# Kernel optimization log

Hardware: AMD Instinct MI355X
Metric: run time of the kernel (lower is better)

Reference implementation:

```python
import jax, jax.numpy as jnp
import numpy as np

CHANNEL = 512
EDGE_F = 30
NB, NA = 16, 128


def setup_inputs() -> dict:
    key = jax.random.key(0)
    ks = jax.random.split(key, 8)
    h = jax.random.normal(ks[0], (NB, NA, CHANNEL), dtype=jnp.float32)
    e = jax.random.normal(ks[1], (NB, NA, NA, EDGE_F), dtype=jnp.float32)
    node_mask = jax.random.randint(ks[2], (NB, NA, 1), 0, 2).astype(jnp.float32)
    edge_mask = jax.random.randint(ks[3], (NB, NA, NA, 1), 0, 2).astype(jnp.float32)
    # Linear params (torch convention: y = x @ W.T + b), kaiming-uniform-ish scale
    lim_f = 1.0 / np.sqrt(EDGE_F)
    filter_W = jax.random.uniform(ks[4], (CHANNEL, EDGE_F), jnp.float32, -lim_f, lim_f)
    filter_b = jax.random.uniform(ks[5], (CHANNEL,), jnp.float32, -lim_f, lim_f)
    lim_w = 1.0 / np.sqrt(2 * CHANNEL)
    w_W = jax.random.uniform(ks[6], (CHANNEL, 2 * CHANNEL), jnp.float32, -lim_w, lim_w)
    w_b = jax.random.uniform(ks[7], (CHANNEL,), jnp.float32, -lim_w, lim_w)
    return {"h": h, "e": e, "node_mask": node_mask, "edge_mask": edge_mask,
            "filter_W": filter_W, "filter_b": filter_b, "w_W": w_W, "w_b": w_b}


def reference(h, e, node_mask, edge_mask, filter_W, filter_b, w_W, w_b):
    # edge filter: Linear(30 -> C) + SELU, masked  -> (n_b, n_a, n_a, C)
    ef = jax.nn.selu(jnp.einsum('bijf,cf->bijc', e, filter_W) + filter_b) * edge_mask
    # h1[b,i,c] = sum_j h[b,j,c] * ef[b,i,j,c]   (masked sum aggregation)
    h1 = jnp.einsum('bjc,bijc->bic', h, ef)
    # node MLP on concat([h, h1]) + SELU, masked, residual
    z = jnp.concatenate([h, h1], axis=-1)  # (n_b, n_a, 2C)
    h1 = jax.nn.selu(jnp.einsum('bid,cd->bic', z, w_W) + w_b) * node_mask
    return h1 + h
```

## Files before the change

### kernel.cpp

```cpp
#include <hip/hip_runtime.h>
#include <hip/hip_bf16.h>
#include <math.h>

#define NBATCH 16
#define NA     128
#define CH     512
#define EFEAT  30

typedef __attribute__((ext_vector_type(8))) short          bf16x8;
typedef __attribute__((ext_vector_type(4))) float          f32x4;
typedef __attribute__((ext_vector_type(8))) unsigned short ushort8;
typedef __attribute__((ext_vector_type(4))) unsigned short ushort4_t;

__device__ __forceinline__ float selu_f(float x) {
    const float SA = 1.7580993408473766f;
    float e = __expf(x);
    return x > 0.0f ? 1.0507009873554805f * x : fmaf(SA, e, -SA);
}

__device__ __forceinline__ unsigned short f2bf(float f) {
    __hip_bfloat16 h = __float2bfloat16(f);
    return *reinterpret_cast<unsigned short*>(&h);
}

__global__ __launch_bounds__(256, 4)
void k_edge_mfma(const float* __restrict__ h, const float* __restrict__ e,
                 const float* __restrict__ node_mask, const float* __restrict__ edge_mask,
                 const float* __restrict__ fW, const float* __restrict__ fb,
                 unsigned short* __restrict__ z)
{
    __shared__ unsigned short e_lds[NA * 40];
    __shared__ int   jlist[NA];
    __shared__ int   wcnt[2];

    const int row = (blockIdx.x & 7) * 256 + (blockIdx.x >> 3);
    if (node_mask[row] == 0.0f) return;
    const int b = row >> 7;

    const int tid  = threadIdx.x;
    const int lane = tid & 63;
    const int wv   = tid >> 6;
    const int s    = lane & 15;
    const int g    = lane >> 4;
    const int cbase = wv * 128;

    float myq = 0.0f; unsigned long long bl = 0;
    if (tid < NA) {
        myq = edge_mask[(size_t)row * NA + tid];
        bl = __ballot(myq != 0.0f);
        if ((tid & 63) == 0) wcnt[tid >> 6] = __popcll(bl);
    }
    __syncthreads();
    const int nlive  = wcnt[0] + wcnt[1];
    const int ntiles = (nlive + 15) >> 4;
    if (tid < NA) {
        if (myq != 0.0f) {
            const int base = (tid >= 64) ? wcnt[0] : 0;
            const int pos  = __popcll(bl & ((1ull << (tid & 63)) - 1));
            jlist[base + pos] = tid;
        }
        if (tid >= nlive) jlist[tid] = 0;
    }
    __syncthreads();

    bf16x8 afrag[8];
    #pragma unroll
    for (int cf = 0; cf < 8; ++cf) {
        const int c = cbase + cf * 16 + s;
        const float* wrow = fW + (size_t)c * EFEAT;
        ushort8 t;
        #pragma unroll
        for (int e8 = 0; e8 < 8; ++e8) {
            const int k = g * 8 + e8;
            const float v = (k < EFEAT) ? wrow[k] : (k == EFEAT ? fb[c] : 0.0f);
            t[e8] = f2bf(v);
        }
        afrag[cf] = *(bf16x8*)&t;
    }

    const float* esrc = e + (size_t)row * (NA * EFEAT);
    const int npad = ntiles * 16;
    for (int idx = tid; idx < npad * 32; idx += 256) {
        const int p = idx >> 5, f = idx & 31;
        float v = 0.0f;
        if (p < nlive) {
            const int j = jlist[p];
            v = (f < EFEAT) ? esrc[j * EFEAT + f] : (f == EFEAT ? 1.0f : 0.0f);
        }
        e_lds[p * 40 + f] = f2bf(v);
    }

    unsigned short* zrow = z + (size_t)row * (2 * CH);
    const float* hrow = h + (size_t)row * CH;
    zrow[tid]       = f2bf(hrow[tid]);
    zrow[tid + 256] = f2bf(hrow[tid + 256]);

    __syncthreads();

    f32x4 acc[8];
    #pragma unroll
    for (int cf = 0; cf < 8; ++cf) acc[cf] = (f32x4){0.f, 0.f, 0.f, 0.f};

    #pragma unroll 2
    for (int jt = 0; jt < ntiles; ++jt) {
        const int   p   = jt * 16 + s;
        const float emj = (p < nlive) ? 1.0f : 0.0f;
        const int   jj  = jlist[p];
        const bf16x8 bfrag = *(const bf16x8*)&e_lds[p * 40 + g * 8];
        const float* hbase = h + ((size_t)(b * NA) + jj) * CH;
        f32x4 hv[8];
        #pragma unroll
        for (int cf = 0; cf < 8; ++cf)
            hv[cf] = *(const f32x4*)&hbase[cbase + cf * 16 + g * 4];
        #pragma unroll
        for (int cf = 0; cf < 8; ++cf) {
            f32x4 S = __builtin_amdgcn_mfma_f32_16x16x32_bf16(
                          afrag[cf], bfrag, (f32x4){0.f, 0.f, 0.f, 0.f}, 0, 0, 0);
            #pragma unroll
            for (int q = 0; q < 4; ++q) {
                const float sv = selu_f(S[q]);
                acc[cf][q] = fmaf(emj, sv * hv[cf][q], acc[cf][q]);
            }
        }
    }

    #pragma unroll
    for (int m = 1; m <= 8; m <<= 1)
        #pragma unroll
        for (int cf = 0; cf < 8; ++cf)
            #pragma unroll
            for (int q = 0; q < 4; ++q)
                acc[cf][q] += __shfl_xor(acc[cf][q], m, 64);

    if (s == 0) {
        #pragma unroll
        for (int cf = 0; cf < 8; ++cf) {
            const int c0 = cbase + cf * 16 + g * 4;
            ushort4_t o;
            #pragma unroll
            for (int q = 0; q < 4; ++q) o[q] = f2bf(acc[cf][q]);
            *(ushort4_t*)&zrow[CH + c0] = o;
        }
    }
}

__global__ __launch_bounds__(256, 4)
void k_node_mlp(const float* __restrict__ h, const unsigned short* __restrict__ z,
                const float* __restrict__ node_mask,
                const float* __restrict__ wW, const float* __restrict__ wb,
                float* __restrict__ out)
{
    __shared__ short As[32][136];
    __shared__ short Bs[32][136];
    const int tid = threadIdx.x;
    const int bid = (blockIdx.x & 7) * 128 + (blockIdx.x >> 3);
    const int m0  = (bid >> 4) * 32;
    const int n0  = (bid & 15) * 32;
    const int lane = tid & 63, wv = tid >> 6;
    const int wr = wv >> 1, wc = wv & 1;
    const int s  = lane & 15, g = lane >> 4;

    const int arow = tid >> 3;
    const int akb  = (tid & 7) * 16;

    f32x4 acc = {0.f, 0.f, 0.f, 0.f};

    for (int ks = 0; ks < 2 * CH; ks += 128) {
        const ushort8 a0 = *(const ushort8*)&z[(size_t)(m0 + arow) * (2 * CH) + ks + akb];
        const ushort8 a1 = *(const ushort8*)&z[(size_t)(m0 + arow) * (2 * CH) + ks + akb + 8];
        const float* wsrc = wW + (size_t)(n0 + arow) * (2 * CH) + ks + akb;
        const f32x4 u0 = *(const f32x4*)&wsrc[0];
        const f32x4 u1 = *(const f32x4*)&wsrc[4];
        const f32x4 u2 = *(const f32x4*)&wsrc[8];
        const f32x4 u3 = *(const f32x4*)&wsrc[12];
        ushort8 t0, t1;
        #pragma unroll
        for (int q = 0; q < 4; ++q) {
            t0[q] = f2bf(u0[q]); t0[q + 4] = f2bf(u1[q]);
            t1[q] = f2bf(u2[q]); t1[q + 4] = f2bf(u3[q]);
        }
        *(ushort8*)&As[arow][akb]     = a0;
        *(ushort8*)&As[arow][akb + 8] = a1;
        *(ushort8*)&Bs[arow][akb]     = t0;
        *(ushort8*)&Bs[arow][akb + 8] = t1;
        __syncthreads();
        #pragma unroll
        for (int kk = 0; kk < 128; kk += 32) {
            const bf16x8 af = *(const bf16x8*)&As[wr * 16 + s][kk + g * 8];
            const bf16x8 bf = *(const bf16x8*)&Bs[wc * 16 + s][kk + g * 8];
            acc = __builtin_amdgcn_mfma_f32_16x16x32_bf16(af, bf, acc, 0, 0, 0);
        }
        __syncthreads();
    }

    const int r0 = m0 + wr * 16 + g * 4;
    const int c  = n0 + wc * 16 + s;
    const float wbv = wb[c];
    const f32x4 nmv = *(const f32x4*)&node_mask[r0];
    #pragma unroll
    for (int q = 0; q < 4; ++q) {
        const size_t gi = (size_t)(r0 + q) * CH + c;
        out[gi] = selu_f(acc[q] + wbv) * nmv[q] + h[gi];
    }
}

extern "C" void kernel_launch(void* const* d_in, const int* in_sizes, int n_in,
                              void* d_out, int out_size, void* d_ws, size_t ws_size,
                              hipStream_t stream)
{
    (void)in_sizes; (void)n_in; (void)out_size; (void)ws_size;
    const float* h  = (const float*)d_in[0];
    const float* e  = (const float*)d_in[1];
    const float* nm = (const float*)d_in[2];
    const float* em = (const float*)d_in[3];
    const float* fW = (const float*)d_in[4];
    const float* fb = (const float*)d_in[5];
    const float* wW = (const float*)d_in[6];
    const float* wb = (const float*)d_in[7];
    float* out = (float*)d_out;
    unsigned short* z = (unsigned short*)d_ws;

    k_edge_mfma<<<NBATCH * NA, 256, 0, stream>>>(h, e, nm, em, fW, fb, z);
    k_node_mlp<<<(NBATCH * NA / 32) * (CH / 32), 256, 0, stream>>>(h, z, nm, wW, wb, out);
}
```

Before: 137.6 us.

## Pre-convert MLP weights to bf16, stage full edge row contiguously, drop LDS in GEMM

A new kernel converts w_W to bf16 once per call, so the node-MLP GEMM can read bf16 fragments directly from global memory with no LDS tiling or barriers. In the edge kernel, the whole e row is loaded with coalesced float4 reads into LDS at its natural j index. This load overlaps with the mask ballot and the filter-weight fragment setup, which removes one barrier phase and the scattered gather through jlist. In exchange it adds a kernel launch, loads edges even for masked-out j, and the GEMM now relies on the cache instead of LDS reuse.

```diff
diff --git a/kernel.cpp b/kernel.cpp
--- a/kernel.cpp
+++ b/kernel.cpp
@@ -21,6 +21,16 @@
 __device__ __forceinline__ unsigned short f2bf(float f) {
     __hip_bfloat16 h = __float2bfloat16(f);
     return *reinterpret_cast<unsigned short*>(&h);
+}
+
+__global__ __launch_bounds__(256)
+void k_cvt_w(const float* __restrict__ wW, unsigned short* __restrict__ wWb)
+{
+    const int i = (blockIdx.x * 256 + threadIdx.x) * 4;
+    const f32x4 v = *(const f32x4*)&wW[i];
+    ushort4_t o;
+    o.x = f2bf(v[0]); o.y = f2bf(v[1]); o.z = f2bf(v[2]); o.w = f2bf(v[3]);
+    *(ushort4_t*)&wWb[i] = o;
 }
 
 __global__ __launch_bounds__(256, 4)
@@ -50,6 +60,48 @@
         bl = __ballot(myq != 0.0f);
         if ((tid & 63) == 0) wcnt[tid >> 6] = __popcll(bl);
     }
+
+    const f32x4* esrc4 = (const f32x4*)(e + (size_t)row * (NA * EFEAT));
+    #pragma unroll
+    for (int it = 0; it < 4; ++it) {
+        const int v4 = tid + it * 256;
+        if (v4 < 960) {
+            const f32x4 x = esrc4[v4];
+            const int flat = v4 * 4;
+            #pragma unroll
+            for (int u = 0; u < 4; ++u) {
+                const int fl = flat + u;
+                const int j  = fl / 30;
+                const int f  = fl - j * 30;
+                e_lds[j * 40 + f] = f2bf(x[u]);
+            }
+        }
+    }
+    if (tid < NA) {
+        e_lds[tid * 40 + 30] = f2bf(1.0f);
+        e_lds[tid * 40 + 31] = 0;
+    }
+
+    bf16x8 afrag[8];
+    #pragma unroll
+    for (int cf = 0; cf < 8; ++cf) {
+        const int c = cbase + cf * 16 + s;
+        const float* wrow = fW + (size_t)c * EFEAT;
+        ushort8 t;
+        #pragma unroll
+        for (int e8 = 0; e8 < 8; ++e8) {
+            const int k = g * 8 + e8;
+            const float v = (k < EFEAT) ? wrow[k] : (k == EFEAT ? fb[c] : 0.0f);
+            t[e8] = f2bf(v);
+        }
+        afrag[cf] = *(bf16x8*)&t;
+    }
+
+    unsigned short* zrow = z + (size_t)row * (2 * CH);
+    const float* hrow = h + (size_t)row * CH;
+    zrow[tid]       = f2bf(hrow[tid]);
+    zrow[tid + 256] = f2bf(hrow[tid + 256]);
+
     __syncthreads();
     const int nlive  = wcnt[0] + wcnt[1];
     const int ntiles = (nlive + 15) >> 4;
@@ -63,40 +115,6 @@
     }
     __syncthreads();
 
-    bf16x8 afrag[8];
-    #pragma unroll
-    for (int cf = 0; cf < 8; ++cf) {
-        const int c = cbase + cf * 16 + s;
-        const float* wrow = fW + (size_t)c * EFEAT;
-        ushort8 t;
-        #pragma unroll
-        for (int e8 = 0; e8 < 8; ++e8) {
-            const int k = g * 8 + e8;
-            const float v = (k < EFEAT) ? wrow[k] : (k == EFEAT ? fb[c] : 0.0f);
-            t[e8] = f2bf(v);
-        }
-        afrag[cf] = *(bf16x8*)&t;
-    }
-
-    const float* esrc = e + (size_t)row * (NA * EFEAT);
-    const int npad = ntiles * 16;
-    for (int idx = tid; idx < npad * 32; idx += 256) {
-        const int p = idx >> 5, f = idx & 31;
-        float v = 0.0f;
-        if (p < nlive) {
-            const int j = jlist[p];
-            v = (f < EFEAT) ? esrc[j * EFEAT + f] : (f == EFEAT ? 1.0f : 0.0f);
-        }
-        e_lds[p * 40 + f] = f2bf(v);
-    }
-
-    unsigned short* zrow = z + (size_t)row * (2 * CH);
-    const float* hrow = h + (size_t)row * CH;
-    zrow[tid]       = f2bf(hrow[tid]);
-    zrow[tid + 256] = f2bf(hrow[tid + 256]);
-
-    __syncthreads();
-
     f32x4 acc[8];
     #pragma unroll
     for (int cf = 0; cf < 8; ++cf) acc[cf] = (f32x4){0.f, 0.f, 0.f, 0.f};
@@ -106,7 +124,7 @@
         const int   p   = jt * 16 + s;
         const float emj = (p < nlive) ? 1.0f : 0.0f;
         const int   jj  = jlist[p];
-        const bf16x8 bfrag = *(const bf16x8*)&e_lds[p * 40 + g * 8];
+        const bf16x8 bfrag = *(const bf16x8*)&e_lds[jj * 40 + g * 8];
         const float* hbase = h + ((size_t)(b * NA) + jj) * CH;
         f32x4 hv[8];
         #pragma unroll
@@ -147,50 +165,27 @@
 __global__ __launch_bounds__(256, 4)
 void k_node_mlp(const float* __restrict__ h, const unsigned short* __restrict__ z,
                 const float* __restrict__ node_mask,
-                const float* __restrict__ wW, const float* __restrict__ wb,
+                const unsigned short* __restrict__ wWb, const float* __restrict__ wb,
                 float* __restrict__ out)
 {
-    __shared__ short As[32][136];
-    __shared__ short Bs[32][136];
-    const int tid = threadIdx.x;
-    const int bid = (blockIdx.x & 7) * 128 + (blockIdx.x >> 3);
-    const int m0  = (bid >> 4) * 32;
-    const int n0  = (bid & 15) * 32;
+    const int tid  = threadIdx.x;
+    const int bid  = (blockIdx.x & 7) * 128 + (blockIdx.x >> 3);
+    const int m0   = (bid >> 4) * 32;
+    const int n0   = (bid & 15) * 32;
     const int lane = tid & 63, wv = tid >> 6;
     const int wr = wv >> 1, wc = wv & 1;
     const int s  = lane & 15, g = lane >> 4;
 
-    const int arow = tid >> 3;
-    const int akb  = (tid & 7) * 16;
+    const unsigned short* A0 = z   + (size_t)(m0 + wr * 16 + s) * (2 * CH) + g * 8;
+    const unsigned short* B0 = wWb + (size_t)(n0 + wc * 16 + s) * (2 * CH) + g * 8;
 
     f32x4 acc = {0.f, 0.f, 0.f, 0.f};
 
-    for (int ks = 0; ks < 2 * CH; ks += 128) {
-        const ushort8 a0 = *(const ushort8*)&z[(size_t)(m0 + arow) * (2 * CH) + ks + akb];
-        const ushort8 a1 = *(const ushort8*)&z[(size_t)(m0 + arow) * (2 * CH) + ks + akb + 8];
-        const float* wsrc = wW + (size_t)(n0 + arow) * (2 * CH) + ks + akb;
-        const f32x4 u0 = *(const f32x4*)&wsrc[0];
-        const f32x4 u1 = *(const f32x4*)&wsrc[4];
-        const f32x4 u2 = *(const f32x4*)&wsrc[8];
-        const f32x4 u3 = *(const f32x4*)&wsrc[12];
-        ushort8 t0, t1;
-        #pragma unroll
-        for (int q = 0; q < 4; ++q) {
-            t0[q] = f2bf(u0[q]); t0[q + 4] = f2bf(u1[q]);
-            t1[q] = f2bf(u2[q]); t1[q + 4] = f2bf(u3[q]);
-        }
-        *(ushort8*)&As[arow][akb]     = a0;
-        *(ushort8*)&As[arow][akb + 8] = a1;
-        *(ushort8*)&Bs[arow][akb]     = t0;
-        *(ushort8*)&Bs[arow][akb + 8] = t1;
-        __syncthreads();
-        #pragma unroll
-        for (int kk = 0; kk < 128; kk += 32) {
-            const bf16x8 af = *(const bf16x8*)&As[wr * 16 + s][kk + g * 8];
-            const bf16x8 bf = *(const bf16x8*)&Bs[wc * 16 + s][kk + g * 8];
-            acc = __builtin_amdgcn_mfma_f32_16x16x32_bf16(af, bf, acc, 0, 0, 0);
-        }
-        __syncthreads();
+    #pragma unroll 4
+    for (int ks = 0; ks < 2 * CH; ks += 32) {
+        const bf16x8 a = *(const bf16x8*)&A0[ks];
+        const bf16x8 bfr = *(const bf16x8*)&B0[ks];
+        acc = __builtin_amdgcn_mfma_f32_16x16x32_bf16(a, bfr, acc, 0, 0, 0);
     }
 
     const int r0 = m0 + wr * 16 + g * 4;
@@ -218,8 +213,10 @@
     const float* wW = (const float*)d_in[6];
     const float* wb = (const float*)d_in[7];
     float* out = (float*)d_out;
-    unsigned short* z = (unsigned short*)d_ws;
-
+    unsigned short* z   = (unsigned short*)d_ws;
+    unsigned short* wWb = (unsigned short*)d_ws + 2048*1024;
+
+    k_cvt_w<<<512, 256, 0, stream>>>(wW, wWb);
     k_edge_mfma<<<NBATCH * NA, 256, 0, stream>>>(h, e, nm, em, fW, fb, z);
-    k_node_mlp<<<(NBATCH * NA / 32) * (CH / 32), 256, 0, stream>>>(h, z, nm, wW, wb, out);
-}
+    k_node_mlp<<<(NBATCH * NA / 32) * (CH / 32), 256, 0, stream>>>(h, z, nm, wWb, wb, out);
+}
```

After: 155.2 us. +12.8%, slower.

## Drop edge compaction and LDS staging; load edge features directly into MFMA fragments

Applied to the files above, without the earlier changes.

Removes the per-row ballot/prefix compaction of live edges and the LDS staging of edge features. Each lane now builds its B fragment straight from global memory with vectorized float2 loads, and all 128 neighbors are processed with the edge mask applied as a multiplier. This drops two block barriers and the LDS round-trip. In exchange the kernel no longer skips masked-out edges, so roughly twice as many MFMA, SELU and h loads are executed.

```diff
diff --git a/kernel.cpp b/kernel.cpp
--- a/kernel.cpp
+++ b/kernel.cpp
@@ -9,6 +9,7 @@
 
 typedef __attribute__((ext_vector_type(8))) short          bf16x8;
 typedef __attribute__((ext_vector_type(4))) float          f32x4;
+typedef __attribute__((ext_vector_type(2))) float          f32x2;
 typedef __attribute__((ext_vector_type(8))) unsigned short ushort8;
 typedef __attribute__((ext_vector_type(4))) unsigned short ushort4_t;
 
@@ -21,6 +22,24 @@
 __device__ __forceinline__ unsigned short f2bf(float f) {
     __hip_bfloat16 h = __float2bfloat16(f);
     return *reinterpret_cast<unsigned short*>(&h);
+}
+
+__device__ __forceinline__ bf16x8 load_row30(const float* __restrict__ base,
+                                             int g, float slot30) {
+    ushort8 t;
+    const f32x2 p0 = *(const f32x2*)(base + g * 8 + 0);
+    const f32x2 p1 = *(const f32x2*)(base + g * 8 + 2);
+    const f32x2 p2 = *(const f32x2*)(base + g * 8 + 4);
+    t[0] = f2bf(p0.x); t[1] = f2bf(p0.y);
+    t[2] = f2bf(p1.x); t[3] = f2bf(p1.y);
+    t[4] = f2bf(p2.x); t[5] = f2bf(p2.y);
+    if (g < 3) {
+        const f32x2 p3 = *(const f32x2*)(base + g * 8 + 6);
+        t[6] = f2bf(p3.x); t[7] = f2bf(p3.y);
+    } else {
+        t[6] = f2bf(slot30); t[7] = 0;
+    }
+    return *(bf16x8*)&t;
 }
 
 __global__ __launch_bounds__(256, 4)
@@ -29,10 +48,6 @@
                  const float* __restrict__ fW, const float* __restrict__ fb,
                  unsigned short* __restrict__ z)
 {
-    __shared__ unsigned short e_lds[NA * 40];
-    __shared__ int   jlist[NA];
-    __shared__ int   wcnt[2];
-
     const int row = (blockIdx.x & 7) * 256 + (blockIdx.x >> 3);
     if (node_mask[row] == 0.0f) return;
     const int b = row >> 7;
@@ -44,50 +59,11 @@
     const int g    = lane >> 4;
     const int cbase = wv * 128;
 
-    float myq = 0.0f; unsigned long long bl = 0;
-    if (tid < NA) {
-        myq = edge_mask[(size_t)row * NA + tid];
-        bl = __ballot(myq != 0.0f);
-        if ((tid & 63) == 0) wcnt[tid >> 6] = __popcll(bl);
-    }
-    __syncthreads();
-    const int nlive  = wcnt[0] + wcnt[1];
-    const int ntiles = (nlive + 15) >> 4;
-    if (tid < NA) {
-        if (myq != 0.0f) {
-            const int base = (tid >= 64) ? wcnt[0] : 0;
-            const int pos  = __popcll(bl & ((1ull << (tid & 63)) - 1));
-            jlist[base + pos] = tid;
-        }
-        if (tid >= nlive) jlist[tid] = 0;
-    }
-    __syncthreads();
-
     bf16x8 afrag[8];
     #pragma unroll
     for (int cf = 0; cf < 8; ++cf) {
         const int c = cbase + cf * 16 + s;
-        const float* wrow = fW + (size_t)c * EFEAT;
-        ushort8 t;
-        #pragma unroll
-        for (int e8 = 0; e8 < 8; ++e8) {
-            const int k = g * 8 + e8;
-            const float v = (k < EFEAT) ? wrow[k] : (k == EFEAT ? fb[c] : 0.0f);
-            t[e8] = f2bf(v);
-        }
-        afrag[cf] = *(bf16x8*)&t;
-    }
-
-    const float* esrc = e + (size_t)row * (NA * EFEAT);
-    const int npad = ntiles * 16;
-    for (int idx = tid; idx < npad * 32; idx += 256) {
-        const int p = idx >> 5, f = idx & 31;
-        float v = 0.0f;
-        if (p < nlive) {
-            const int j = jlist[p];
-            v = (f < EFEAT) ? esrc[j * EFEAT + f] : (f == EFEAT ? 1.0f : 0.0f);
-        }
-        e_lds[p * 40 + f] = f2bf(v);
+        afrag[cf] = load_row30(fW + (size_t)c * EFEAT, g, fb[c]);
     }
 
     unsigned short* zrow = z + (size_t)row * (2 * CH);
@@ -95,23 +71,23 @@
     zrow[tid]       = f2bf(hrow[tid]);
     zrow[tid + 256] = f2bf(hrow[tid + 256]);
 
-    __syncthreads();
+    const float* erow = e + (size_t)row * (NA * EFEAT);
+    const float* emrow = edge_mask + (size_t)row * NA;
 
     f32x4 acc[8];
     #pragma unroll
     for (int cf = 0; cf < 8; ++cf) acc[cf] = (f32x4){0.f, 0.f, 0.f, 0.f};
 
     #pragma unroll 2
-    for (int jt = 0; jt < ntiles; ++jt) {
-        const int   p   = jt * 16 + s;
-        const float emj = (p < nlive) ? 1.0f : 0.0f;
-        const int   jj  = jlist[p];
-        const bf16x8 bfrag = *(const bf16x8*)&e_lds[p * 40 + g * 8];
-        const float* hbase = h + ((size_t)(b * NA) + jj) * CH;
+    for (int jt = 0; jt < 8; ++jt) {
+        const int j = jt * 16 + s;
+        const float emj = emrow[j];
+        const bf16x8 bfrag = load_row30(erow + (size_t)j * EFEAT, g, 1.0f);
+        const float* hbase = h + ((size_t)(b * NA) + j) * CH + cbase;
         f32x4 hv[8];
         #pragma unroll
         for (int cf = 0; cf < 8; ++cf)
-            hv[cf] = *(const f32x4*)&hbase[cbase + cf * 16 + g * 4];
+            hv[cf] = *(const f32x4*)&hbase[cf * 16 + g * 4];
         #pragma unroll
         for (int cf = 0; cf < 8; ++cf) {
             f32x4 S = __builtin_amdgcn_mfma_f32_16x16x32_bf16(
```

Result: slower. 213.0 us (+54.8%).
